# Performance work log

Measured on AMD Instinct MI355X. Metric: run time of the kernel, lower is better.

Reference implementation:

```python
import jax, jax.numpy as jnp
import numpy as np

B, N, C, K = 32, 4096, 768, 8

def setup_inputs() -> dict:
    key = jax.random.key(0)
    ks = jax.random.split(key, 5)
    x = jax.random.normal(ks[0], (B, N, C), dtype=jnp.float32)
    ln_gamma = jnp.ones((C,), dtype=jnp.float32)
    ln_beta = jnp.zeros((C,), dtype=jnp.float32)
    W1 = jax.random.normal(ks[1], (C, C), dtype=jnp.float32) / np.sqrt(C)
    b1 = jnp.zeros((C,), dtype=jnp.float32)
    W2 = jax.random.normal(ks[2], (C, K), dtype=jnp.float32) / np.sqrt(C)
    b2 = jnp.zeros((K,), dtype=jnp.float32)
    return {"x": x, "ln_gamma": ln_gamma, "ln_beta": ln_beta,
            "W1": W1, "b1": b1, "W2": W2, "b2": b2}

def reference(x, ln_gamma, ln_beta, W1, b1, W2, b2):
    # LayerNorm over last dim (eps matches torch default 1e-5)
    mu = jnp.mean(x, axis=-1, keepdims=True)
    var = jnp.mean(jnp.square(x - mu), axis=-1, keepdims=True)
    h = (x - mu) * jax.lax.rsqrt(var + 1e-5) * ln_gamma + ln_beta
    # Linear -> exact GELU -> Linear
    h = jax.nn.gelu(h @ W1 + b1, approximate=False)
    logits = h @ W2 + b2  # [B, N, K]
    # softmax over tokens (dim=1)
    attn = jax.nn.softmax(logits, axis=1)
    # weighted token pooling: [B,N,K],[B,N,C] -> [B,K,C]
    return jnp.einsum('bnk,bnc->bkc', attn, x)
```

## Files before the change

kernel.cpp:

```cpp
#include <hip/hip_runtime.h>
#include <hip/hip_fp16.h>

#define M_TOKENS (32*4096)
#define C_DIM 768
#define K_OUT 8

typedef _Float16 f16x8 __attribute__((ext_vector_type(8)));
typedef float f32x4 __attribute__((ext_vector_type(4)));

__device__ __forceinline__ void gl2lds16(const void* g, void* l) {
    __builtin_amdgcn_global_load_lds((const __attribute__((address_space(1))) void*)g,
                                     (__attribute__((address_space(3))) void*)l, 16, 0, 0);
}

__device__ __forceinline__ float gelu_fast(float x) {
    const float z  = x * 0.70710678118654752440f;
    const float az = fabsf(z);
    const float t  = __builtin_amdgcn_rcpf(1.0f + 0.3275911f * az);
    float p = 1.061405429f;
    p = p * t - 1.453152027f;
    p = p * t + 1.421413741f;
    p = p * t - 0.284496736f;
    p = p * t + 0.254829592f;
    p = p * t;
    const float e = __expf(-az * az);
    const float erf_abs = 1.0f - p * e;
    const float erf_z = copysignf(erf_abs, z);
    return 0.5f * x * (1.0f + erf_z);
}

__global__ __launch_bounds__(256) void prep_w1(const float* __restrict__ w1,
                                               const float* __restrict__ gamma,
                                               _Float16* __restrict__ w1t) {
    __shared__ float t[64][65];
    const int k0 = blockIdx.x * 64, n0 = blockIdx.y * 64;
    const int c = threadIdx.x & 63, r4 = threadIdx.x >> 6;
#pragma unroll
    for (int p = 0; p < 16; ++p) {
        const int r = p*4 + r4;
        t[r][c] = w1[(size_t)(k0 + r)*C_DIM + n0 + c];
    }
    __syncthreads();
    const float g = gamma[k0 + c];
#pragma unroll
    for (int p = 0; p < 16; ++p) {
        const int n = p*4 + r4;
        w1t[(size_t)(n0 + n)*C_DIM + k0 + c] = (_Float16)(t[c][n] * g);
    }
}

__global__ __launch_bounds__(256) void prep_b1(const float* __restrict__ w1,
                                               const float* __restrict__ beta,
                                               const float* __restrict__ b1,
                                               float* __restrict__ b1p) {
    __shared__ float red[256];
    const int nl = threadIdx.x & 63;
    const int n = blockIdx.x*64 + nl;
    const int part = threadIdx.x >> 6;
    float s = 0.f;
    for (int k = part*192; k < part*192 + 192; ++k)
        s += beta[k] * w1[(size_t)k*C_DIM + n];
    red[threadIdx.x] = s;
    __syncthreads();
    if (part == 0)
        b1p[n] = b1[n] + red[nl] + red[nl+64] + red[nl+128] + red[nl+192];
}

__global__ __launch_bounds__(256) void xnorm_kernel(const float* __restrict__ x,
                                                    _Float16* __restrict__ xn) {
    const int row0 = blockIdx.x*8 + (threadIdx.x >> 6)*2;
    const int lane = threadIdx.x & 63;
    const float4* xr0 = (const float4*)(x + (size_t)row0 * C_DIM);
    const float4* xr1 = (const float4*)(x + (size_t)(row0 + 1) * C_DIM);
    float4 v0[3], v1[3];
#pragma unroll
    for (int i = 0; i < 3; ++i) { v0[i] = xr0[lane + i*64]; v1[i] = xr1[lane + i*64]; }
    float sa = 0.f, s2a = 0.f, sb = 0.f, s2b = 0.f;
#pragma unroll
    for (int i = 0; i < 3; ++i) {
        sa  += v0[i].x + v0[i].y + v0[i].z + v0[i].w;
        s2a += v0[i].x*v0[i].x + v0[i].y*v0[i].y + v0[i].z*v0[i].z + v0[i].w*v0[i].w;
        sb  += v1[i].x + v1[i].y + v1[i].z + v1[i].w;
        s2b += v1[i].x*v1[i].x + v1[i].y*v1[i].y + v1[i].z*v1[i].z + v1[i].w*v1[i].w;
    }
#pragma unroll
    for (int m = 1; m < 64; m <<= 1) {
        sa += __shfl_xor(sa, m); s2a += __shfl_xor(s2a, m);
        sb += __shfl_xor(sb, m); s2b += __shfl_xor(s2b, m);
    }
    const float mua = sa * (1.f/768.f);
    const float rsa = rsqrtf(s2a * (1.f/768.f) - mua*mua + 1e-5f);
    const float nma = -mua * rsa;
    const float mub = sb * (1.f/768.f);
    const float rsb = rsqrtf(s2b * (1.f/768.f) - mub*mub + 1e-5f);
    const float nmb = -mub * rsb;
    _Float16* xo0 = xn + (size_t)row0 * C_DIM;
    _Float16* xo1 = xn + (size_t)(row0 + 1) * C_DIM;
#pragma unroll
    for (int i = 0; i < 3; ++i) {
        union { _Float16 h[4]; uint2 uu; } pk;
        pk.h[0] = (_Float16)(v0[i].x*rsa + nma);
        pk.h[1] = (_Float16)(v0[i].y*rsa + nma);
        pk.h[2] = (_Float16)(v0[i].z*rsa + nma);
        pk.h[3] = (_Float16)(v0[i].w*rsa + nma);
        *(uint2*)(xo0 + (size_t)(lane + i*64)*4) = pk.uu;
        pk.h[0] = (_Float16)(v1[i].x*rsb + nmb);
        pk.h[1] = (_Float16)(v1[i].y*rsb + nmb);
        pk.h[2] = (_Float16)(v1[i].z*rsb + nmb);
        pk.h[3] = (_Float16)(v1[i].w*rsb + nmb);
        *(uint2*)(xo1 + (size_t)(lane + i*64)*4) = pk.uu;
    }
}

__global__ __launch_bounds__(256) void gemm1_h_kernel(const _Float16* __restrict__ xn,
        const _Float16* __restrict__ w1t, const float* __restrict__ b1p,
        const float* __restrict__ w2, float* __restrict__ logits) {
    __shared__ __align__(16) union {
        struct { _Float16 a[128*64]; _Float16 b[128*64]; } s;
        _Float16 ht[128*136];
    } u;
    __shared__ float w2s[128*K_OUT];
    __shared__ float b1s[128];

    const int tid = threadIdx.x;
    const int wid = tid >> 6, lane = tid & 63;
    const int l15 = lane & 15, q = lane >> 4;
    const int wm = wid >> 1, wn = wid & 1;

    const int L = blockIdx.y * 6 + blockIdx.x;
    const int swz = (L & 7) * 768 + (L >> 3);
    const int n0 = (swz % 6) * 128;
    const int m0 = (swz / 6) * 128;

    for (int i = tid; i < 128*K_OUT; i += 256) w2s[i] = w2[(size_t)n0*K_OUT + i];
    if (tid < 128) b1s[tid] = b1p[n0 + tid];

    f32x4 acc[4][4] = {};

    for (int kt = 0; kt < 12; ++kt) {
        const int k0 = kt * 64;
#pragma unroll
        for (int i = 0; i < 4; ++i) {
            const int Li = i*256 + tid;
            const int row = Li >> 3, j = (Li & 7) ^ (row & 7);
            gl2lds16(xn + (size_t)(m0 + row)*C_DIM + k0 + j*8,
                     &u.s.a[(i*256 + wid*64)*8]);
        }
#pragma unroll
        for (int i = 0; i < 4; ++i) {
            const int Li = i*256 + tid;
            const int row = Li >> 3, j = (Li & 7) ^ (row & 7);
            gl2lds16(w1t + (size_t)(n0 + row)*C_DIM + k0 + j*8,
                     &u.s.b[(i*256 + wid*64)*8]);
        }
        __syncthreads();
#pragma unroll
        for (int kk = 0; kk < 2; ++kk) {
            f16x8 af[4], bfr[4];
#pragma unroll
            for (int nt = 0; nt < 4; ++nt) {
                const int row = wn*64 + nt*16 + l15;
                const int j = (kk*4 + q) ^ (row & 7);
                af[nt] = *(const f16x8*)&u.s.b[row*64 + j*8];
            }
#pragma unroll
            for (int mt = 0; mt < 4; ++mt) {
                const int row = wm*64 + mt*16 + l15;
                const int j = (kk*4 + q) ^ (row & 7);
                bfr[mt] = *(const f16x8*)&u.s.a[row*64 + j*8];
            }
#pragma unroll
            for (int nt = 0; nt < 4; ++nt)
#pragma unroll
                for (int mt = 0; mt < 4; ++mt)
                    acc[nt][mt] = __builtin_amdgcn_mfma_f32_16x16x32_f16(
                        af[nt], bfr[mt], acc[nt][mt], 0, 0, 0);
        }
        __syncthreads();
    }

#pragma unroll
    for (int nt = 0; nt < 4; ++nt) {
#pragma unroll
        for (int mt = 0; mt < 4; ++mt) {
            const int token = wm*64 + mt*16 + l15;
            const int nl = wn*64 + nt*16 + q*4;
            union { _Float16 h[4]; uint2 uu; } pk;
#pragma unroll
            for (int r = 0; r < 4; ++r)
                pk.h[r] = (_Float16)gelu_fast(acc[nt][mt][r] + b1s[nl + r]);
            *(uint2*)&u.ht[token*136 + nl] = pk.uu;
        }
    }
    __syncthreads();

    f16x8 wf[4];
#pragma unroll
    for (int ks = 0; ks < 4; ++ks) {
        f16x8 t;
#pragma unroll
        for (int j = 0; j < 8; ++j) {
            const int kd = ks*32 + q*8 + j;
            t[j] = (_Float16)((l15 < K_OUT) ? w2s[kd*K_OUT + l15] : 0.f);
        }
        wf[ks] = t;
    }
#pragma unroll
    for (int t2 = 0; t2 < 2; ++t2) {
        const int tt = wid*2 + t2;
        f32x4 p = {};
#pragma unroll
        for (int ks = 0; ks < 4; ++ks) {
            const f16x8 a = *(const f16x8*)&u.ht[(tt*16 + l15)*136 + ks*32 + q*8];
            p = __builtin_amdgcn_mfma_f32_16x16x32_f16(a, wf[ks], p, 0, 0, 0);
        }
        if (l15 < K_OUT) {
#pragma unroll
            for (int r = 0; r < 4; ++r)
                atomicAdd(&logits[(size_t)(m0 + tt*16 + q*4 + r)*K_OUT + l15], p[r]);
        }
    }
}


__global__ __launch_bounds__(256) void stats_kernel(const float* __restrict__ x,
                                                    float2* __restrict__ stats) {
    const int row = blockIdx.x*4 + (threadIdx.x >> 6);
    const int lane = threadIdx.x & 63;
    const float4* xr = (const float4*)(x + (size_t)row * C_DIM);
    float s = 0.f, s2 = 0.f;
#pragma unroll
    for (int i = 0; i < 3; ++i) {
        const float4 v = xr[lane + i*64];
        s  += v.x + v.y + v.z + v.w;
        s2 += v.x*v.x + v.y*v.y + v.z*v.z + v.w*v.w;
    }
#pragma unroll
    for (int m = 1; m < 64; m <<= 1) { s += __shfl_xor(s, m); s2 += __shfl_xor(s2, m); }
    if (lane == 0) {
        const float mu = s * (1.f/768.f);
        const float rs = rsqrtf(s2 * (1.f/768.f) - mu*mu + 1e-5f);
        stats[row] = make_float2(rs, -mu*rs);
    }
}

__global__ __launch_bounds__(256) void gemm1_ln_kernel(const float* __restrict__ x,
        const float2* __restrict__ stats, const _Float16* __restrict__ w1t,
        const float* __restrict__ b1p, const float* __restrict__ w2,
        float* __restrict__ logits) {
    __shared__ __align__(16) union {
        struct { float a[128*64]; _Float16 b[128*64]; } s;
        _Float16 ht[128*136];
    } u;
    __shared__ float w2s[128*K_OUT];
    __shared__ float b1s[128];

    const int tid = threadIdx.x;
    const int wid = tid >> 6, lane = tid & 63;
    const int l15 = lane & 15, q = lane >> 4;
    const int wm = wid >> 1, wn = wid & 1;
    const int n0 = blockIdx.x * 128;
    const int m0 = blockIdx.y * 128;

    for (int i = tid; i < 128*K_OUT; i += 256) w2s[i] = w2[(size_t)n0*K_OUT + i];
    if (tid < 128) b1s[tid] = b1p[n0 + tid];

    float rsL[4], nmL[4];
#pragma unroll
    for (int mt = 0; mt < 4; ++mt) {
        const float2 st = stats[m0 + wm*64 + mt*16 + l15];
        rsL[mt] = st.x; nmL[mt] = st.y;
    }

    f32x4 acc[4][4] = {};

    for (int kt = 0; kt < 12; ++kt) {
        const int k0 = kt * 64;
#pragma unroll
        for (int i = 0; i < 8; ++i) {
            const int L = i*256 + tid;
            const int row = L >> 4, g = (L & 15) ^ (row & 15);
            gl2lds16(x + (size_t)(m0 + row)*C_DIM + k0 + g*4,
                     &u.s.a[(i*256 + wid*64)*4]);
        }
#pragma unroll
        for (int i = 0; i < 4; ++i) {
            const int L = i*256 + tid;
            const int row = L >> 3, j = (L & 7) ^ (row & 7);
            gl2lds16(w1t + (size_t)(n0 + row)*C_DIM + k0 + j*8,
                     &u.s.b[(i*256 + wid*64)*8]);
        }
        __syncthreads();
#pragma unroll
        for (int kk = 0; kk < 2; ++kk) {
            f16x8 af[4], bfr[4];
#pragma unroll
            for (int nt = 0; nt < 4; ++nt) {
                const int row = wn*64 + nt*16 + l15;
                const int j = (kk*4 + q) ^ (row & 7);
                af[nt] = *(const f16x8*)&u.s.b[row*64 + j*8];
            }
#pragma unroll
            for (int mt = 0; mt < 4; ++mt) {
                const int row = wm*64 + mt*16 + l15;
                const int gc = kk*8 + q*2;
                const int c0 = gc ^ (row & 15), c1 = (gc + 1) ^ (row & 15);
                const f32x4 v0 = *(const f32x4*)&u.s.a[row*64 + c0*4];
                const f32x4 v1 = *(const f32x4*)&u.s.a[row*64 + c1*4];
                f16x8 t;
#pragma unroll
                for (int j = 0; j < 4; ++j) {
                    t[j]   = (_Float16)(v0[j]*rsL[mt] + nmL[mt]);
                    t[4+j] = (_Float16)(v1[j]*rsL[mt] + nmL[mt]);
                }
                bfr[mt] = t;
            }
#pragma unroll
            for (int nt = 0; nt < 4; ++nt)
#pragma unroll
                for (int mt = 0; mt < 4; ++mt)
                    acc[nt][mt] = __builtin_amdgcn_mfma_f32_16x16x32_f16(
                        af[nt], bfr[mt], acc[nt][mt], 0, 0, 0);
        }
        __syncthreads();
    }

#pragma unroll
    for (int nt = 0; nt < 4; ++nt) {
#pragma unroll
        for (int mt = 0; mt < 4; ++mt) {
            const int token = wm*64 + mt*16 + l15;
            const int nl = wn*64 + nt*16 + q*4;
            union { _Float16 h[4]; uint2 uu; } pk;
#pragma unroll
            for (int r = 0; r < 4; ++r)
                pk.h[r] = (_Float16)gelu_fast(acc[nt][mt][r] + b1s[nl + r]);
            *(uint2*)&u.ht[token*136 + nl] = pk.uu;
        }
    }
    __syncthreads();

    f16x8 wf[4];
#pragma unroll
    for (int ks = 0; ks < 4; ++ks) {
        f16x8 t;
#pragma unroll
        for (int j = 0; j < 8; ++j) {
            const int kd = ks*32 + q*8 + j;
            t[j] = (_Float16)((l15 < K_OUT) ? w2s[kd*K_OUT + l15] : 0.f);
        }
        wf[ks] = t;
    }
#pragma unroll
    for (int t2 = 0; t2 < 2; ++t2) {
        const int tt = wid*2 + t2;
        f32x4 p = {};
#pragma unroll
        for (int ks = 0; ks < 4; ++ks) {
            const f16x8 a = *(const f16x8*)&u.ht[(tt*16 + l15)*136 + ks*32 + q*8];
            p = __builtin_amdgcn_mfma_f32_16x16x32_f16(a, wf[ks], p, 0, 0, 0);
        }
        if (l15 < K_OUT) {
#pragma unroll
            for (int r = 0; r < 4; ++r)
                atomicAdd(&logits[(size_t)(m0 + tt*16 + q*4 + r)*K_OUT + l15], p[r]);
        }
    }
}

__global__ __launch_bounds__(256) void softmax_kernel(float* p) {
    const int b = blockIdx.x >> 3, k = blockIdx.x & 7;
    const size_t base = ((size_t)b*4096)*K_OUT + k;
    const int tid = threadIdx.x;
    float r[16];
    float mx = -1e30f;
#pragma unroll
    for (int i = 0; i < 16; ++i) {
        r[i] = p[base + (size_t)(tid + i*256)*K_OUT];
        mx = fmaxf(mx, r[i]);
    }
#pragma unroll
    for (int m = 1; m < 64; m <<= 1) mx = fmaxf(mx, __shfl_xor(mx, m));
    __shared__ float redm[4], reds[4];
    if ((tid & 63) == 0) redm[tid >> 6] = mx;
    __syncthreads();
    mx = fmaxf(fmaxf(redm[0], redm[1]), fmaxf(redm[2], redm[3]));
    float s = 0.f;
#pragma unroll
    for (int i = 0; i < 16; ++i) { r[i] = __expf(r[i] - mx); s += r[i]; }
#pragma unroll
    for (int m = 1; m < 64; m <<= 1) s += __shfl_xor(s, m);
    if ((tid & 63) == 0) reds[tid >> 6] = s;
    __syncthreads();
    s = reds[0] + reds[1] + reds[2] + reds[3];
    const float inv = 1.f / s;
#pragma unroll
    for (int i = 0; i < 16; ++i)
        p[base + (size_t)(tid + i*256)*K_OUT] = r[i] * inv;
}

__global__ __launch_bounds__(192) void pool_kernel(const float* __restrict__ x,
        const float* __restrict__ attn, float* __restrict__ out) {
    const int b = blockIdx.x, nc = blockIdx.y;
    const int t0 = nc * 128;
    __shared__ float as_[128*K_OUT];
    for (int i = threadIdx.x; i < 128*K_OUT; i += 192)
        as_[i] = attn[((size_t)b*4096 + t0)*K_OUT + i];
    __syncthreads();
    const int c = threadIdx.x * 4;
    float acc[K_OUT][4] = {};
    const float* xb = x + ((size_t)b*4096 + t0)*C_DIM + c;
#pragma unroll 4
    for (int i = 0; i < 128; ++i) {
        const float4 xv = *(const float4*)(xb + (size_t)i*C_DIM);
#pragma unroll
        for (int k = 0; k < K_OUT; ++k) {
            const float a = as_[i*K_OUT + k];
            acc[k][0] += a*xv.x; acc[k][1] += a*xv.y;
            acc[k][2] += a*xv.z; acc[k][3] += a*xv.w;
        }
    }
#pragma unroll
    for (int k = 0; k < K_OUT; ++k)
#pragma unroll
        for (int j = 0; j < 4; ++j)
            atomicAdd(&out[((size_t)b*K_OUT + k)*C_DIM + c + j], acc[k][j]);
}

extern "C" void kernel_launch(void* const* d_in, const int* in_sizes, int n_in,
                              void* d_out, int out_size, void* d_ws, size_t ws_size,
                              hipStream_t stream) {
    const float* x     = (const float*)d_in[0];
    const float* gamma = (const float*)d_in[1];
    const float* beta  = (const float*)d_in[2];
    const float* W1    = (const float*)d_in[3];
    const float* b1    = (const float*)d_in[4];
    const float* W2    = (const float*)d_in[5];
    (void)in_sizes; (void)n_in;

    float* out = (float*)d_out;
    char* ws = (char*)d_ws;

    const size_t XN_BYTES  = (size_t)M_TOKENS * C_DIM * 2;
    const size_t NEED_NEW  = XN_BYTES + 1179648 + 4096 + 4194304;

    if (ws_size >= NEED_NEW) {
        _Float16* xn     = (_Float16*)ws;
        _Float16* w1t    = (_Float16*)(ws + XN_BYTES);
        float*    b1p    = (float*)(ws + XN_BYTES + 1179648);
        float*    logits = (float*)(ws + XN_BYTES + 1179648 + 4096);

        (void)hipMemsetAsync(logits, 0, (size_t)M_TOKENS * K_OUT * 4, stream);
        (void)hipMemsetAsync(d_out, 0, (size_t)out_size * sizeof(float), stream);

        prep_w1<<<dim3(12, 12), 256, 0, stream>>>(W1, gamma, w1t);
        prep_b1<<<12, 256, 0, stream>>>(W1, beta, b1, b1p);
        xnorm_kernel<<<M_TOKENS/8, 256, 0, stream>>>(x, xn);
        gemm1_h_kernel<<<dim3(6, 1024), 256, 0, stream>>>(xn, w1t, b1p, W2, logits);
        softmax_kernel<<<256, 256, 0, stream>>>(logits);
        pool_kernel<<<dim3(32, 32), 192, 0, stream>>>(x, logits, out);
    } else {
        float2*   stats  = (float2*)ws;
        _Float16* w1t    = (_Float16*)(ws + 1048576);
        float*    b1p    = (float*)(ws + 2228224);
        float*    logits = (float*)(ws + 2232320);

        (void)hipMemsetAsync(logits, 0, (size_t)M_TOKENS * K_OUT * 4, stream);
        (void)hipMemsetAsync(d_out, 0, (size_t)out_size * sizeof(float), stream);

        prep_w1<<<dim3(12, 12), 256, 0, stream>>>(W1, gamma, w1t);
        prep_b1<<<12, 256, 0, stream>>>(W1, beta, b1, b1p);
        stats_kernel<<<M_TOKENS/4, 256, 0, stream>>>(x, stats);
        gemm1_ln_kernel<<<dim3(6, 1024), 256, 0, stream>>>(x, stats, w1t, b1p, W2, logits);
        softmax_kernel<<<256, 256, 0, stream>>>(logits);
        pool_kernel<<<dim3(32, 32), 192, 0, stream>>>(x, logits, out);
    }
}
```

Baseline: 1.006 ms.

## Precompute GEMM address offsets, add occupancy hint, fuse softmax normalization into pool

The GEMM kernel now computes global source pointers and swizzled LDS offsets once, outside the k-loop, and advances them by pointer increments. It also gets a launch_bounds occupancy hint of 4 blocks. The softmax kernel now writes only per-(batch,k) max and inverse sum, and the pool kernel applies exp and scaling while loading logits. This removes the normalized-probability write pass and cuts address arithmetic in the GEMM inner loop, at the cost of possible register pressure from the occupancy bound.

```diff
diff --git a/kernel.cpp b/kernel.cpp
--- a/kernel.cpp
+++ b/kernel.cpp
@@ -112,7 +112,7 @@
     }
 }
 
-__global__ __launch_bounds__(256) void gemm1_h_kernel(const _Float16* __restrict__ xn,
+__global__ __launch_bounds__(256, 4) void gemm1_h_kernel(const _Float16* __restrict__ xn,
         const _Float16* __restrict__ w1t, const float* __restrict__ b1p,
         const float* __restrict__ w2, float* __restrict__ logits) {
     __shared__ __align__(16) union {
@@ -135,40 +135,46 @@
     for (int i = tid; i < 128*K_OUT; i += 256) w2s[i] = w2[(size_t)n0*K_OUT + i];
     if (tid < 128) b1s[tid] = b1p[n0 + tid];
 
+    const _Float16* asrc[4];
+    const _Float16* bsrc[4];
+#pragma unroll
+    for (int i = 0; i < 4; ++i) {
+        const int Li = i*256 + tid;
+        const int row = Li >> 3, j = (Li & 7) ^ (row & 7);
+        asrc[i] = xn  + (size_t)(m0 + row)*C_DIM + j*8;
+        bsrc[i] = w1t + (size_t)(n0 + row)*C_DIM + j*8;
+    }
+    int afo[4], bfo[4];
+#pragma unroll
+    for (int t = 0; t < 4; ++t) {
+        const int rb = wn*64 + t*16 + l15;
+        afo[t] = rb*128 + ((q ^ (rb & 7)) << 4);
+        const int rm = wm*64 + t*16 + l15;
+        bfo[t] = rm*128 + ((q ^ (rm & 7)) << 4);
+    }
+    const char* sa = (const char*)u.s.a;
+    const char* sb = (const char*)u.s.b;
+
     f32x4 acc[4][4] = {};
 
     for (int kt = 0; kt < 12; ++kt) {
-        const int k0 = kt * 64;
 #pragma unroll
         for (int i = 0; i < 4; ++i) {
-            const int Li = i*256 + tid;
-            const int row = Li >> 3, j = (Li & 7) ^ (row & 7);
-            gl2lds16(xn + (size_t)(m0 + row)*C_DIM + k0 + j*8,
-                     &u.s.a[(i*256 + wid*64)*8]);
-        }
-#pragma unroll
-        for (int i = 0; i < 4; ++i) {
-            const int Li = i*256 + tid;
-            const int row = Li >> 3, j = (Li & 7) ^ (row & 7);
-            gl2lds16(w1t + (size_t)(n0 + row)*C_DIM + k0 + j*8,
-                     &u.s.b[(i*256 + wid*64)*8]);
+            gl2lds16(asrc[i], (void*)&u.s.a[(i*256 + wid*64)*8]);
+            gl2lds16(bsrc[i], (void*)&u.s.b[(i*256 + wid*64)*8]);
+            asrc[i] += 64; bsrc[i] += 64;
         }
         __syncthreads();
 #pragma unroll
         for (int kk = 0; kk < 2; ++kk) {
+            const int kx = kk * 64;
             f16x8 af[4], bfr[4];
 #pragma unroll
-            for (int nt = 0; nt < 4; ++nt) {
-                const int row = wn*64 + nt*16 + l15;
-                const int j = (kk*4 + q) ^ (row & 7);
-                af[nt] = *(const f16x8*)&u.s.b[row*64 + j*8];
-            }
-#pragma unroll
-            for (int mt = 0; mt < 4; ++mt) {
-                const int row = wm*64 + mt*16 + l15;
-                const int j = (kk*4 + q) ^ (row & 7);
-                bfr[mt] = *(const f16x8*)&u.s.a[row*64 + j*8];
-            }
+            for (int nt = 0; nt < 4; ++nt)
+                af[nt] = *(const f16x8*)(sb + (afo[nt] ^ kx));
+#pragma unroll
+            for (int mt = 0; mt < 4; ++mt)
+                bfr[mt] = *(const f16x8*)(sa + (bfo[mt] ^ kx));
 #pragma unroll
             for (int nt = 0; nt < 4; ++nt)
 #pragma unroll
@@ -368,7 +374,8 @@
     }
 }
 
-__global__ __launch_bounds__(256) void softmax_kernel(float* p) {
+__global__ __launch_bounds__(256) void lse_kernel(const float* __restrict__ p,
+                                                  float2* __restrict__ st) {
     const int b = blockIdx.x >> 3, k = blockIdx.x & 7;
     const size_t base = ((size_t)b*4096)*K_OUT + k;
     const int tid = threadIdx.x;
@@ -387,25 +394,25 @@
     mx = fmaxf(fmaxf(redm[0], redm[1]), fmaxf(redm[2], redm[3]));
     float s = 0.f;
 #pragma unroll
-    for (int i = 0; i < 16; ++i) { r[i] = __expf(r[i] - mx); s += r[i]; }
+    for (int i = 0; i < 16; ++i) s += __expf(r[i] - mx);
 #pragma unroll
     for (int m = 1; m < 64; m <<= 1) s += __shfl_xor(s, m);
     if ((tid & 63) == 0) reds[tid >> 6] = s;
     __syncthreads();
     s = reds[0] + reds[1] + reds[2] + reds[3];
-    const float inv = 1.f / s;
-#pragma unroll
-    for (int i = 0; i < 16; ++i)
-        p[base + (size_t)(tid + i*256)*K_OUT] = r[i] * inv;
+    if (tid == 0) st[blockIdx.x] = make_float2(mx, 1.f / s);
 }
 
 __global__ __launch_bounds__(192) void pool_kernel(const float* __restrict__ x,
-        const float* __restrict__ attn, float* __restrict__ out) {
+        const float* __restrict__ logits, const float2* __restrict__ st,
+        float* __restrict__ out) {
     const int b = blockIdx.x, nc = blockIdx.y;
     const int t0 = nc * 128;
     __shared__ float as_[128*K_OUT];
-    for (int i = threadIdx.x; i < 128*K_OUT; i += 192)
-        as_[i] = attn[((size_t)b*4096 + t0)*K_OUT + i];
+    for (int i = threadIdx.x; i < 128*K_OUT; i += 192) {
+        const float2 mk = st[b*K_OUT + (i & 7)];
+        as_[i] = __expf(logits[((size_t)b*4096 + t0)*K_OUT + i] - mk.x) * mk.y;
+    }
     __syncthreads();
     const int c = threadIdx.x * 4;
     float acc[K_OUT][4] = {};
@@ -442,37 +449,40 @@
     char* ws = (char*)d_ws;
 
     const size_t XN_BYTES  = (size_t)M_TOKENS * C_DIM * 2;
-    const size_t NEED_NEW  = XN_BYTES + 1179648 + 4096 + 4194304;
+    const size_t LOG_BYTES = (size_t)M_TOKENS * K_OUT * 4;
+    const size_t NEED_NEW  = XN_BYTES + 1179648 + 4096 + LOG_BYTES + 2048;
 
     if (ws_size >= NEED_NEW) {
         _Float16* xn     = (_Float16*)ws;
         _Float16* w1t    = (_Float16*)(ws + XN_BYTES);
         float*    b1p    = (float*)(ws + XN_BYTES + 1179648);
         float*    logits = (float*)(ws + XN_BYTES + 1179648 + 4096);
-
-        (void)hipMemsetAsync(logits, 0, (size_t)M_TOKENS * K_OUT * 4, stream);
+        float2*   st2    = (float2*)(ws + XN_BYTES + 1179648 + 4096 + LOG_BYTES);
+
+        (void)hipMemsetAsync(logits, 0, LOG_BYTES, stream);
         (void)hipMemsetAsync(d_out, 0, (size_t)out_size * sizeof(float), stream);
 
         prep_w1<<<dim3(12, 12), 256, 0, stream>>>(W1, gamma, w1t);
         prep_b1<<<12, 256, 0, stream>>>(W1, beta, b1, b1p);
         xnorm_kernel<<<M_TOKENS/8, 256, 0, stream>>>(x, xn);
         gemm1_h_kernel<<<dim3(6, 1024), 256, 0, stream>>>(xn, w1t, b1p, W2, logits);
-        softmax_kernel<<<256, 256, 0, stream>>>(logits);
-        pool_kernel<<<dim3(32, 32), 192, 0, stream>>>(x, logits, out);
+        lse_kernel<<<256, 256, 0, stream>>>(logits, st2);
+        pool_kernel<<<dim3(32, 32), 192, 0, stream>>>(x, logits, st2, out);
     } else {
         float2*   stats  = (float2*)ws;
         _Float16* w1t    = (_Float16*)(ws + 1048576);
         float*    b1p    = (float*)(ws + 2228224);
         float*    logits = (float*)(ws + 2232320);
-
-        (void)hipMemsetAsync(logits, 0, (size_t)M_TOKENS * K_OUT * 4, stream);
+        float2*   st2    = (float2*)(ws + 2232320 + LOG_BYTES);
+
+        (void)hipMemsetAsync(logits, 0, LOG_BYTES, stream);
         (void)hipMemsetAsync(d_out, 0, (size_t)out_size * sizeof(float), stream);
 
         prep_w1<<<dim3(12, 12), 256, 0, stream>>>(W1, gamma, w1t);
         prep_b1<<<12, 256, 0, stream>>>(W1, beta, b1, b1p);
         stats_kernel<<<M_TOKENS/4, 256, 0, stream>>>(x, stats);
         gemm1_ln_kernel<<<dim3(6, 1024), 256, 0, stream>>>(x, stats, w1t, b1p, W2, logits);
-        softmax_kernel<<<256, 256, 0, stream>>>(logits);
-        pool_kernel<<<dim3(32, 32), 192, 0, stream>>>(x, logits, out);
-    }
-}
+        lse_kernel<<<256, 256, 0, stream>>>(logits, st2);
+        pool_kernel<<<dim3(32, 32), 192, 0, stream>>>(x, logits, st2, out);
+    }
+}
```

New measurement: 1.053 ms. 4.7% more time.
